# Optimization experiments

Hardware: AMD Instinct MI355X
Metric: run time of the kernel (lower is better)

## Reference

```python
import jax, jax.numpy as jnp
import numpy as np

N = 100000   # nodes per type (equal so the module's sloppy self-indexing is valid)
E = 1600000  # edges, avg degree 16
DIN = 128    # input feature dim (lazily inferred by SAGEConv((-1,-1), ...))
H = 256      # hidden (init default)


def _w(k, i, o):
    return jax.random.normal(k, (i, o), jnp.float32) * (1.0 / np.sqrt(i))


def setup_inputs() -> dict:
    key = jax.random.key(0)
    ks = jax.random.split(key, 16)
    inp = {
        "x_human": jax.random.normal(ks[0], (N, DIN), jnp.float32),
        "x_bact": jax.random.normal(ks[1], (N, DIN), jnp.float32),
        "edge_index": jax.random.randint(ks[2], (2, E), 0, N, dtype=jnp.int32),
        # human branch conv1 (DIN->H) and conv2 (H->H)
        "h1_Wl": _w(ks[3], DIN, H), "h1_Wr": _w(ks[4], DIN, H), "h1_b": jnp.zeros((H,), jnp.float32),
        "h2_Wl": _w(ks[5], H, H),   "h2_Wr": _w(ks[6], H, H),   "h2_b": jnp.zeros((H,), jnp.float32),
        # bacterial branch conv1 (DIN->H) and conv2 (H->H)
        "b1_Wl": _w(ks[7], DIN, H), "b1_Wr": _w(ks[8], DIN, H), "b1_b": jnp.zeros((H,), jnp.float32),
        "b2_Wl": _w(ks[9], H, H),   "b2_Wr": _w(ks[10], H, H),  "b2_b": jnp.zeros((H,), jnp.float32),
    }
    return inp


def sage_conv(x, src, dst, Wl, Wr, b):
    """PyG SAGEConv (aggr='mean', root_weight=True):
    out = Linear(mean_{j in N(i)} x_j) + Linear_noBias(x_i).
    Aggregate first, then matmul (same op order as PyG => less FLOPs/traffic)."""
    s = jax.ops.segment_sum(x[src], dst, num_segments=N)          # [N, d] scatter-sum of gathered messages
    cnt = jax.ops.segment_sum(jnp.ones((src.shape[0],), x.dtype), dst, num_segments=N)
    agg = s / jnp.maximum(cnt, 1.0)[:, None]                      # mean; isolated nodes -> 0
    return agg @ Wl + x @ Wr + b


def reference(x_human, x_bact, edge_index,
              h1_Wl, h1_Wr, h1_b, h2_Wl, h2_Wr, h2_b,
              b1_Wl, b1_Wr, b1_b, b2_Wl, b2_Wr, b2_b):
    src, dst = edge_index[0], edge_index[1]   # human -> bacterial
    # rev = edge.flip(0): messages flow bacterial_id -> human_id
    h = jax.nn.relu(sage_conv(x_human, dst, src, h1_Wl, h1_Wr, h1_b))
    h = jax.nn.relu(sage_conv(h, dst, src, h2_Wl, h2_Wr, h2_b))
    b = jax.nn.relu(sage_conv(x_bact, src, dst, b1_Wl, b1_Wr, b1_b))
    b = jax.nn.relu(sage_conv(b, src, dst, b2_Wl, b2_Wr, b2_b))
    return h, b
```

## Files before the change

### kernel.cpp

```cpp
#include <hip/hip_runtime.h>
#include <stdint.h>

using short8  = __attribute__((ext_vector_type(8))) short;
using float4v = __attribute__((ext_vector_type(4))) float;

__device__ __forceinline__ float b2f(unsigned short u) {
    union { unsigned int i; float f; } v; v.i = ((unsigned int)u) << 16; return v.f;
}
__device__ __forceinline__ unsigned short f2b(float f) {
    union { float f; unsigned int i; } v; v.f = f;
    unsigned int x = v.i;
    unsigned int r = (x + 0x7fffu + ((x >> 16) & 1u)) >> 16;
    return (unsigned short)r;
}

__device__ __forceinline__ void gload_lds16(const void* g, void* l) {
    __builtin_amdgcn_global_load_lds((const __attribute__((address_space(1))) void*)g,
                                     (__attribute__((address_space(3))) void*)l, 16, 0, 0);
}

__global__ __launch_bounds__(256)
void fill_ell_ranged(const int* __restrict__ src, const int* __restrict__ dst,
                     int* __restrict__ cnt_h, int* __restrict__ cnt_b,
                     int* __restrict__ adj_h, int* __restrict__ adj_b,
                     int E, int N, int nch) {
    const int NR = 8;
    int r     = blockIdx.x & (NR - 1);
    int chunk = blockIdx.x >> 3;
    int rng = (N + NR - 1) / NR;
    int lo = r * rng;
    int hi = lo + rng; if (hi > N) hi = N;
    int per = (E + nch - 1) / nch;
    int e0 = chunk * per;
    int e1 = e0 + per; if (e1 > E) e1 = E;
    for (int e = e0 + (int)threadIdx.x; e < e1; e += 256) {
        int s = __builtin_nontemporal_load(src + e);
        int d = __builtin_nontemporal_load(dst + e);
        if (s >= lo && s < hi) {
            int sl = atomicAdd(cnt_h + s, 1);
            if (sl < 64) adj_h[((size_t)s << 6) + sl] = d;
        }
        if (d >= lo && d < hi) {
            int sl = atomicAdd(cnt_b + d, 1);
            if (sl < 64) adj_b[((size_t)d << 6) + sl] = s;
        }
    }
}

__global__ void count_deg(const int* __restrict__ src, const int* __restrict__ dst,
                          int* __restrict__ deg_h, int* __restrict__ deg_b, int E) {
    int e = blockIdx.x * blockDim.x + threadIdx.x;
    if (e < E) {
        int s = __builtin_nontemporal_load(src + e);
        int d = __builtin_nontemporal_load(dst + e);
        atomicAdd(deg_h + s, 1);
        atomicAdd(deg_b + d, 1);
    }
}
__global__ void scan1(const int* __restrict__ deg, int* __restrict__ partial, int N) {
    int t = threadIdx.x;
    int base = blockIdx.x * 1024 + t * 4;
    int s = 0;
    #pragma unroll
    for (int i = 0; i < 4; ++i) { int idx = base + i; if (idx < N) s += deg[idx]; }
    #pragma unroll
    for (int off = 32; off; off >>= 1) s += __shfl_down(s, off);
    __shared__ int sm[4];
    if ((t & 63) == 0) sm[t >> 6] = s;
    __syncthreads();
    if (t == 0) partial[blockIdx.x] = sm[0] + sm[1] + sm[2] + sm[3];
}
__global__ void scan2(int* __restrict__ partial, int P) {
    if (blockIdx.x == 0 && threadIdx.x == 0) {
        int run = 0;
        for (int i = 0; i < P; ++i) { int v = partial[i]; partial[i] = run; run += v; }
    }
}
__global__ void scan3(const int* __restrict__ deg, const int* __restrict__ partial,
                      int* __restrict__ row, int N, int E) {
    int t = threadIdx.x;
    int lane = t & 63, wv = t >> 6;
    int base = blockIdx.x * 1024 + t * 4;
    int d[4]; int s = 0;
    #pragma unroll
    for (int i = 0; i < 4; ++i) { int idx = base + i; d[i] = (idx < N) ? deg[idx] : 0; s += d[i]; }
    int inc = s;
    #pragma unroll
    for (int off = 1; off < 64; off <<= 1) { int v = __shfl_up(inc, off); if (lane >= off) inc += v; }
    __shared__ int wsum[4];
    if (lane == 63) wsum[wv] = inc;
    __syncthreads();
    int woff = 0;
    for (int w = 0; w < wv; ++w) woff += wsum[w];
    int run = inc - s + woff + partial[blockIdx.x];
    #pragma unroll
    for (int i = 0; i < 4; ++i) { int idx = base + i; if (idx < N) row[idx] = run; run += d[i]; }
    if (blockIdx.x == 0 && t == 0) row[N] = E;
}
__global__ __launch_bounds__(256)
void fill_adj_ranged(const int* __restrict__ src, const int* __restrict__ dst,
                     int* __restrict__ cur_h, int* __restrict__ cur_b,
                     int* __restrict__ adj_h, int* __restrict__ adj_b,
                     int E, int N, int nch) {
    const int NR = 8;
    int r     = blockIdx.x & (NR - 1);
    int chunk = blockIdx.x >> 3;
    int rng = (N + NR - 1) / NR;
    int lo = r * rng;
    int hi = lo + rng; if (hi > N) hi = N;
    int per = (E + nch - 1) / nch;
    int e0 = chunk * per;
    int e1 = e0 + per; if (e1 > E) e1 = E;
    for (int e = e0 + (int)threadIdx.x; e < e1; e += 256) {
        int s = __builtin_nontemporal_load(src + e);
        int d = __builtin_nontemporal_load(dst + e);
        if (s >= lo && s < hi) adj_h[atomicAdd(cur_h + s, 1)] = d;
        if (d >= lo && d < hi) adj_b[atomicAdd(cur_b + d, 1)] = s;
    }
}

__global__ void cvt_to_bf16(const float* __restrict__ in, unsigned short* __restrict__ out,
                            size_t n4) {
    size_t t = (size_t)blockIdx.x * blockDim.x + threadIdx.x;
    if (t >= n4) return;
    const float4 v = *(const float4*)(in + t * 4);
    ushort4 u;
    u.x = f2b(v.x); u.y = f2b(v.y); u.z = f2b(v.z); u.w = f2b(v.w);
    *(ushort4*)(out + t * 4) = u;
}

template <int D>
__global__ __launch_bounds__(256)
void gather_mean(const unsigned short* __restrict__ x, const int* __restrict__ rowc,
                 const int* __restrict__ adj, unsigned short* __restrict__ out,
                 int N, int ell) {
    constexpr int LPR = D / 8;
    constexpr int G   = 64 / LPR;
    constexpr int UNR = 16 / G;
    int wid  = (blockIdx.x * blockDim.x + threadIdx.x) >> 6;
    int lane = threadIdx.x & 63;
    if (wid >= N) return;
    int beg, deg;
    if (ell) { beg = wid << 6; int c = rowc[wid]; deg = (c < 64) ? c : 64; }
    else     { beg = rowc[wid]; deg = rowc[wid + 1] - beg; }

    const int g  = lane >> (LPR == 16 ? 4 : 5);
    const int gl = lane & (LPR - 1);

    float acc[8];
    #pragma unroll
    for (int p = 0; p < 8; ++p) acc[p] = 0.0f;

    for (int base = 0; base < deg; base += 64) {
        int nb_l = (base + lane < deg) ? adj[beg + base + lane] : 0;
        int m = deg - base; if (m > 64) m = 64;
        int j = 0;
        for (; j + UNR * G <= m; j += UNR * G) {
            int nn[UNR];
            #pragma unroll
            for (int u = 0; u < UNR; ++u) nn[u] = __shfl(nb_l, j + u * G + g);
            short8 vv[UNR];
            #pragma unroll
            for (int u = 0; u < UNR; ++u)
                vv[u] = *(const short8*)(x + (size_t)nn[u] * D + gl * 8);
            #pragma unroll
            for (int u = 0; u < UNR; ++u)
                #pragma unroll
                for (int p = 0; p < 8; ++p) acc[p] += b2f((unsigned short)vv[u][p]);
        }
        for (; j < m; j += G) {
            int idx = j + g;
            int nb = __shfl(nb_l, idx);
            if (idx < m) {
                const short8 v = *(const short8*)(x + (size_t)nb * D + gl * 8);
                #pragma unroll
                for (int p = 0; p < 8; ++p) acc[p] += b2f((unsigned short)v[p]);
            }
        }
    }
    #pragma unroll
    for (int off = LPR; off < 64; off <<= 1) {
        #pragma unroll
        for (int p = 0; p < 8; ++p) acc[p] += __shfl_xor(acc[p], off);
    }
    float inv = 1.0f / (float)((deg > 0) ? deg : 1);
    if (lane < LPR) {
        unsigned short* op = out + (size_t)wid * D + lane * 8;
        short8 u;
        #pragma unroll
        for (int p = 0; p < 8; ++p) u[p] = (short)f2b(acc[p] * inv);
        *(short8*)op = u;
    }
}

__global__ void transpose_w4(const float* __restrict__ W0, const float* __restrict__ W1,
                             const float* __restrict__ W2, const float* __restrict__ W3,
                             unsigned short* __restrict__ T0, unsigned short* __restrict__ T1,
                             unsigned short* __restrict__ T2, unsigned short* __restrict__ T3,
                             int K) {
    int k = blockIdx.x;
    int c = threadIdx.x;
    int m = blockIdx.y;
    const float* W = (m == 0) ? W0 : (m == 1) ? W1 : (m == 2) ? W2 : W3;
    unsigned short* T = (m == 0) ? T0 : (m == 1) ? T1 : (m == 2) ? T2 : T3;
    T[(size_t)c * K + k] = f2b(W[(size_t)k * 256 + c]);
}

template <bool F32OUT>
__global__ __launch_bounds__(256, 3)
void gemm_fused(const unsigned short* __restrict__ A0, const unsigned short* __restrict__ A1,
                const unsigned short* __restrict__ B0, const unsigned short* __restrict__ B1,
                const float* __restrict__ bias,
                float* __restrict__ outf, unsigned short* __restrict__ outb,
                int M, int K) {
    __shared__ unsigned short As[64 * 64];
    __shared__ unsigned short Bs[256 * 64];
    const int tid  = threadIdx.x;
    const int wave = tid >> 6, lane = tid & 63;
    const int wn   = wave;
    const int row0 = blockIdx.x * 64;

    float4v acc[4][4];
    #pragma unroll
    for (int i = 0; i < 4; ++i)
        #pragma unroll
        for (int j = 0; j < 4; ++j) acc[i][j] = (float4v){0.f, 0.f, 0.f, 0.f};

    const int r  = lane >> 3;
    const int cg = lane & 7;
    const int kchunks = K >> 6;
    const int nchunks = kchunks * 2;

    for (int c = 0; c < nchunks; ++c) {
        const unsigned short* Aseg = (c < kchunks) ? A0 : A1;
        const unsigned short* Bseg = (c < kchunks) ? B0 : B1;
        const int k0 = ((c < kchunks) ? c : c - kchunks) << 6;

        if (c) __syncthreads();
        {
            int rr = wave * 16;
            const unsigned short* gp = Aseg + (size_t)(row0 + rr + r) * K + k0 + cg * 8;
            unsigned short* lp = As + rr * 64;
            if (row0 + rr + r < M)     gload_lds16(gp, lp);
            if (row0 + rr + 8 + r < M) gload_lds16(gp + 8 * (size_t)K, lp + 8 * 64);
        }
        {
            int rr = wave * 64;
            const unsigned short* gp = Bseg + (size_t)(rr + r) * K + k0 + cg * 8;
            unsigned short* lp = Bs + rr * 64;
            #pragma unroll
            for (int i = 0; i < 8; ++i)
                gload_lds16(gp + (size_t)(i * 8) * K, lp + i * 8 * 64);
        }
        __syncthreads();

        const int q8 = (lane >> 4) * 8;
        const int l15 = lane & 15;
        #pragma unroll
        for (int kk = 0; kk <= 32; kk += 32) {
            short8 af[4], bf[4];
            #pragma unroll
            for (int f = 0; f < 4; ++f)
                af[f] = *(const short8*)(As + (f * 16 + l15) * 64 + kk + q8);
            #pragma unroll
            for (int f = 0; f < 4; ++f)
                bf[f] = *(const short8*)(Bs + (wn * 64 + f * 16 + l15) * 64 + kk + q8);
            #pragma unroll
            for (int fm = 0; fm < 4; ++fm)
                #pragma unroll
                for (int fn = 0; fn < 4; ++fn)
                    acc[fm][fn] = __builtin_amdgcn_mfma_f32_16x16x32_bf16(
                        af[fm], bf[fn], acc[fm][fn], 0, 0, 0);
        }
    }

    const int l15 = lane & 15;
    const int rq  = (lane >> 4) * 4;
    #pragma unroll
    for (int fn = 0; fn < 4; ++fn) {
        int col = wn * 64 + fn * 16 + l15;
        float bv = bias[col];
        #pragma unroll
        for (int fm = 0; fm < 4; ++fm) {
            #pragma unroll
            for (int rg = 0; rg < 4; ++rg) {
                int row = row0 + fm * 16 + rq + rg;
                if (row < M) {
                    float v = fmaxf(acc[fm][fn][rg] + bv, 0.0f);
                    if (F32OUT) outf[(size_t)row * 256 + col] = v;
                    else        outb[(size_t)row * 256 + col] = f2b(v);
                }
            }
        }
    }
}

extern "C" void kernel_launch(void* const* d_in, const int* in_sizes, int n_in,
                              void* d_out, int out_size, void* d_ws, size_t ws_size,
                              hipStream_t stream) {
    const int DIN = 128, H = 256;
    const int N = in_sizes[0] / DIN;
    const int E = in_sizes[2] / 2;

    const float* xh = (const float*)d_in[0];
    const float* xb = (const float*)d_in[1];
    const int* ei  = (const int*)d_in[2];
    const int* src = ei;
    const int* dst = ei + E;
    const float* h1Wl = (const float*)d_in[3];
    const float* h1Wr = (const float*)d_in[4];
    const float* h1b  = (const float*)d_in[5];
    const float* h2Wl = (const float*)d_in[6];
    const float* h2Wr = (const float*)d_in[7];
    const float* h2b  = (const float*)d_in[8];
    const float* b1Wl = (const float*)d_in[9];
    const float* b1Wr = (const float*)d_in[10];
    const float* b1b  = (const float*)d_in[11];
    const float* b2Wl = (const float*)d_in[12];
    const float* b2Wr = (const float*)d_in[13];
    const float* b2b  = (const float*)d_in[14];

    float* outH = (float*)d_out;
    float* outB = outH + (size_t)N * H;

    const int BLK = 256;
    dim3 blk(BLK);

    const size_t bfElems = (size_t)4 * DIN * H + (size_t)4 * H * H
                         + (size_t)N * DIN + (size_t)2 * N * H;
    const size_t bfBytes = bfElems * 2 + 64;

    const size_t needELL = ((size_t)2 * N + (size_t)128 * N) * 4 + bfBytes;
    const bool useELL = ws_size >= needELL;

    const int* rc_h; const int* rc_b; const int* ajh; const int* ajb;
    uintptr_t intEnd;

    if (useELL) {
        int* cnt_h = (int*)d_ws;
        int* cnt_b = cnt_h + N;
        int* adj_h = cnt_b + N;
        int* adj_b = adj_h + (size_t)N * 64;
        intEnd = (uintptr_t)(adj_b + (size_t)N * 64);

        hipMemsetAsync(cnt_h, 0, (size_t)2 * N * sizeof(int), stream);
        const int NCH = 256;
        fill_ell_ranged<<<dim3(NCH * 8), blk, 0, stream>>>(src, dst, cnt_h, cnt_b,
                                                           adj_h, adj_b, E, N, NCH);
        rc_h = cnt_h; rc_b = cnt_b; ajh = adj_h; ajb = adj_b;
    } else {
        int* deg_h = (int*)d_ws;
        int* deg_b = deg_h + N;
        int* row_h = deg_b + N;
        int* row_b = row_h + (N + 1);
        int* cur_h = row_b + (N + 1);
        int* cur_b = cur_h + N;
        int* partial = cur_b + N;
        int* adj_h = partial + 256;
        int* adj_b = adj_h + E;
        intEnd = (uintptr_t)(adj_b + E);

        const int P = (N + 1023) / 1024;
        hipMemsetAsync(deg_h, 0, (size_t)2 * N * sizeof(int), stream);
        count_deg<<<dim3((E + BLK - 1) / BLK), blk, 0, stream>>>(src, dst, deg_h, deg_b, E);
        scan1<<<dim3(P), blk, 0, stream>>>(deg_h, partial, N);
        scan2<<<dim3(1), blk, 0, stream>>>(partial, P);
        scan3<<<dim3(P), blk, 0, stream>>>(deg_h, partial, row_h, N, E);
        scan1<<<dim3(P), blk, 0, stream>>>(deg_b, partial, N);
        scan2<<<dim3(1), blk, 0, stream>>>(partial, P);
        scan3<<<dim3(P), blk, 0, stream>>>(deg_b, partial, row_b, N, E);
        hipMemcpyAsync(cur_h, row_h, (size_t)N * sizeof(int), hipMemcpyDeviceToDevice, stream);
        hipMemcpyAsync(cur_b, row_b, (size_t)N * sizeof(int), hipMemcpyDeviceToDevice, stream);
        const int NCH = 256;
        fill_adj_ranged<<<dim3(NCH * 8), blk, 0, stream>>>(src, dst, cur_h, cur_b,
                                                           adj_h, adj_b, E, N, NCH);
        rc_h = row_h; rc_b = row_b; ajh = adj_h; ajb = adj_b;
    }
    const int ellf = useELL ? 1 : 0;

    uintptr_t up = (intEnd + 63) & ~(uintptr_t)63;
    unsigned short* wtp = (unsigned short*)up;
    unsigned short* t_h1l = wtp; wtp += DIN * H;
    unsigned short* t_h1r = wtp; wtp += DIN * H;
    unsigned short* t_h2l = wtp; wtp += H * H;
    unsigned short* t_h2r = wtp; wtp += H * H;
    unsigned short* t_b1l = wtp; wtp += DIN * H;
    unsigned short* t_b1r = wtp; wtp += DIN * H;
    unsigned short* t_b2l = wtp; wtp += H * H;
    unsigned short* t_b2r = wtp; wtp += H * H;
    unsigned short* xbf   = wtp;
    unsigned short* aggbf = xbf + (size_t)N * DIN;
    unsigned short* hbf   = aggbf + (size_t)N * H;

    transpose_w4<<<dim3(DIN, 4), blk, 0, stream>>>(h1Wl, h1Wr, b1Wl, b1Wr,
                                                   t_h1l, t_h1r, t_b1l, t_b1r, DIN);
    transpose_w4<<<dim3(H, 4),   blk, 0, stream>>>(h2Wl, h2Wr, b2Wl, b2Wr,
                                                   t_h2l, t_h2r, t_b2l, t_b2r, H);

    dim3 nggrid((N + 3) / 4);
    dim3 ggrid((N + 63) / 64);
    int ncvt = ((size_t)N * DIN / 4 + BLK - 1) / BLK;

    cvt_to_bf16<<<dim3(ncvt), blk, 0, stream>>>(xh, xbf, (size_t)N * DIN / 4);
    gather_mean<128><<<nggrid, blk, 0, stream>>>(xbf, rc_h, ajh, aggbf, N, ellf);
    gemm_fused<false><<<ggrid, blk, 0, stream>>>(aggbf, xbf, t_h1l, t_h1r, h1b,
                                                 nullptr, hbf, N, DIN);
    gather_mean<256><<<nggrid, blk, 0, stream>>>(hbf, rc_h, ajh, aggbf, N, ellf);
    gemm_fused<true><<<ggrid, blk, 0, stream>>>(aggbf, hbf, t_h2l, t_h2r, h2b,
                                                outH, nullptr, N, H);

    cvt_to_bf16<<<dim3(ncvt), blk, 0, stream>>>(xb, xbf, (size_t)N * DIN / 4);
    gather_mean<128><<<nggrid, blk, 0, stream>>>(xbf, rc_b, ajb, aggbf, N, ellf);
    gemm_fused<false><<<ggrid, blk, 0, stream>>>(aggbf, xbf, t_b1l, t_b1r, b1b,
                                                 nullptr, hbf, N, DIN);
    gather_mean<256><<<nggrid, blk, 0, stream>>>(hbf, rc_b, ajb, aggbf, N, ellf);
    gemm_fused<true><<<ggrid, blk, 0, stream>>>(aggbf, hbf, t_b2l, t_b2r, b2b,
                                                outB, nullptr, N, H);
}
```

Before: 1.019 ms.

## Split ELL fill per direction and enlarge GEMM tile to 128 rows

The ELL build kernel is split into two launches, one per direction, each loading the value array only when the key falls in the block's range, which cuts redundant loads and branching. The fused GEMM moves from 64-row tiles with 4 waves to 128-row tiles with 8 waves (2x4 wave grid), so each B tile staged in LDS is reused across twice as many rows. This halves B traffic per output row but raises LDS use per block and changes occupancy, and the ELL build now reads the key array twice.

After: 1.119 ms. 1.1x slower.

```diff
diff --git a/kernel.cpp b/kernel.cpp
--- a/kernel.cpp
+++ b/kernel.cpp
@@ -20,10 +20,9 @@
 }
 
 __global__ __launch_bounds__(256)
-void fill_ell_ranged(const int* __restrict__ src, const int* __restrict__ dst,
-                     int* __restrict__ cnt_h, int* __restrict__ cnt_b,
-                     int* __restrict__ adj_h, int* __restrict__ adj_b,
-                     int E, int N, int nch) {
+void fill_ell_dir(const int* __restrict__ key, const int* __restrict__ val,
+                  int* __restrict__ cnt, int* __restrict__ adj,
+                  int E, int N, int nch) {
     const int NR = 8;
     int r     = blockIdx.x & (NR - 1);
     int chunk = blockIdx.x >> 3;
@@ -34,15 +33,11 @@
     int e0 = chunk * per;
     int e1 = e0 + per; if (e1 > E) e1 = E;
     for (int e = e0 + (int)threadIdx.x; e < e1; e += 256) {
-        int s = __builtin_nontemporal_load(src + e);
-        int d = __builtin_nontemporal_load(dst + e);
-        if (s >= lo && s < hi) {
-            int sl = atomicAdd(cnt_h + s, 1);
-            if (sl < 64) adj_h[((size_t)s << 6) + sl] = d;
-        }
-        if (d >= lo && d < hi) {
-            int sl = atomicAdd(cnt_b + d, 1);
-            if (sl < 64) adj_b[((size_t)d << 6) + sl] = s;
+        int k = __builtin_nontemporal_load(key + e);
+        if (k >= lo && k < hi) {
+            int v = __builtin_nontemporal_load(val + e);
+            int sl = atomicAdd(cnt + k, 1);
+            if (sl < 64) adj[((size_t)k << 6) + sl] = v;
         }
     }
 }
@@ -207,18 +202,19 @@
 }
 
 template <bool F32OUT>
-__global__ __launch_bounds__(256, 3)
+__global__ __launch_bounds__(512, 2)
 void gemm_fused(const unsigned short* __restrict__ A0, const unsigned short* __restrict__ A1,
                 const unsigned short* __restrict__ B0, const unsigned short* __restrict__ B1,
                 const float* __restrict__ bias,
                 float* __restrict__ outf, unsigned short* __restrict__ outb,
                 int M, int K) {
-    __shared__ unsigned short As[64 * 64];
+    __shared__ unsigned short As[128 * 64];
     __shared__ unsigned short Bs[256 * 64];
     const int tid  = threadIdx.x;
     const int wave = tid >> 6, lane = tid & 63;
-    const int wn   = wave;
-    const int row0 = blockIdx.x * 64;
+    const int wm   = wave >> 2;
+    const int wn   = wave & 3;
+    const int row0 = blockIdx.x * 128;
 
     float4v acc[4][4];
     #pragma unroll
@@ -245,11 +241,11 @@
             if (row0 + rr + 8 + r < M) gload_lds16(gp + 8 * (size_t)K, lp + 8 * 64);
         }
         {
-            int rr = wave * 64;
+            int rr = wave * 32;
             const unsigned short* gp = Bseg + (size_t)(rr + r) * K + k0 + cg * 8;
             unsigned short* lp = Bs + rr * 64;
             #pragma unroll
-            for (int i = 0; i < 8; ++i)
+            for (int i = 0; i < 4; ++i)
                 gload_lds16(gp + (size_t)(i * 8) * K, lp + i * 8 * 64);
         }
         __syncthreads();
@@ -261,7 +257,7 @@
             short8 af[4], bf[4];
             #pragma unroll
             for (int f = 0; f < 4; ++f)
-                af[f] = *(const short8*)(As + (f * 16 + l15) * 64 + kk + q8);
+                af[f] = *(const short8*)(As + (wm * 64 + f * 16 + l15) * 64 + kk + q8);
             #pragma unroll
             for (int f = 0; f < 4; ++f)
                 bf[f] = *(const short8*)(Bs + (wn * 64 + f * 16 + l15) * 64 + kk + q8);
@@ -284,7 +280,7 @@
         for (int fm = 0; fm < 4; ++fm) {
             #pragma unroll
             for (int rg = 0; rg < 4; ++rg) {
-                int row = row0 + fm * 16 + rq + rg;
+                int row = row0 + wm * 64 + fm * 16 + rq + rg;
                 if (row < M) {
                     float v = fmaxf(acc[fm][fn][rg] + bv, 0.0f);
                     if (F32OUT) outf[(size_t)row * 256 + col] = v;
@@ -345,8 +341,8 @@
 
         hipMemsetAsync(cnt_h, 0, (size_t)2 * N * sizeof(int), stream);
         const int NCH = 256;
-        fill_ell_ranged<<<dim3(NCH * 8), blk, 0, stream>>>(src, dst, cnt_h, cnt_b,
-                                                           adj_h, adj_b, E, N, NCH);
+        fill_ell_dir<<<dim3(NCH * 8), blk, 0, stream>>>(src, dst, cnt_h, adj_h, E, N, NCH);
+        fill_ell_dir<<<dim3(NCH * 8), blk, 0, stream>>>(dst, src, cnt_b, adj_b, E, N, NCH);
         rc_h = cnt_h; rc_b = cnt_b; ajh = adj_h; ajb = adj_b;
     } else {
         int* deg_h = (int*)d_ws;
@@ -398,22 +394,23 @@
                                                    t_h2l, t_h2r, t_b2l, t_b2r, H);
 
     dim3 nggrid((N + 3) / 4);
-    dim3 ggrid((N + 63) / 64);
+    dim3 ggrid((N + 127) / 128);
+    dim3 gblk(512);
     int ncvt = ((size_t)N * DIN / 4 + BLK - 1) / BLK;
 
     cvt_to_bf16<<<dim3(ncvt), blk, 0, stream>>>(xh, xbf, (size_t)N * DIN / 4);
     gather_mean<128><<<nggrid, blk, 0, stream>>>(xbf, rc_h, ajh, aggbf, N, ellf);
-    gemm_fused<false><<<ggrid, blk, 0, stream>>>(aggbf, xbf, t_h1l, t_h1r, h1b,
-                                                 nullptr, hbf, N, DIN);
+    gemm_fused<false><<<ggrid, gblk, 0, stream>>>(aggbf, xbf, t_h1l, t_h1r, h1b,
+                                                  nullptr, hbf, N, DIN);
     gather_mean<256><<<nggrid, blk, 0, stream>>>(hbf, rc_h, ajh, aggbf, N, ellf);
-    gemm_fused<true><<<ggrid, blk, 0, stream>>>(aggbf, hbf, t_h2l, t_h2r, h2b,
-                                                outH, nullptr, N, H);
+    gemm_fused<true><<<ggrid, gblk, 0, stream>>>(aggbf, hbf, t_h2l, t_h2r, h2b,
+                                                 outH, nullptr, N, H);
 
     cvt_to_bf16<<<dim3(ncvt), blk, 0, stream>>>(xb, xbf, (size_t)N * DIN / 4);
     gather_mean<128><<<nggrid, blk, 0, stream>>>(xbf, rc_b, ajb, aggbf, N, ellf);
-    gemm_fused<false><<<ggrid, blk, 0, stream>>>(aggbf, xbf, t_b1l, t_b1r, b1b,
-                                                 nullptr, hbf, N, DIN);
+    gemm_fused<false><<<ggrid, gblk, 0, stream>>>(aggbf, xbf, t_b1l, t_b1r, b1b,
+                                                  nullptr, hbf, N, DIN);
     gather_mean<256><<<nggrid, blk, 0, stream>>>(hbf, rc_b, ajb, aggbf, N, ellf);
-    gemm_fused<true><<<ggrid, blk, 0, stream>>>(aggbf, hbf, t_b2l, t_b2r, b2b,
-                                                outB, nullptr, N, H);
-}
+    gemm_fused<true><<<ggrid, gblk, 0, stream>>>(aggbf, hbf, t_b2l, t_b2r, b2b,
+                                                 outB, nullptr, N, H);
+}
```

## Interleave human and bacterial branches via fused gemm+gather launches and single prep kernel

Applied to the files above, without the earlier changes.

Merges ELL fill, both bf16 conversions, weight transposes and zero-row setup into one prep kernel. It then runs the two independent branches in lockstep, so each launch pairs one branch's GEMM blocks with the other branch's gather blocks. The gather now loads a full 64-wide adjacency row at once and pads out-of-range lanes with a zero sentinel row instead of using a tail loop. The CSR path is removed. Separate buffers for each branch increase workspace, and a fallback sequential path remains for small workspaces.

Measured after the change: 1.021 ms. No clear change (+0.1%).

```diff
diff --git a/kernel.cpp b/kernel.cpp
--- a/kernel.cpp
+++ b/kernel.cpp
@@ -13,24 +13,22 @@
     unsigned int r = (x + 0x7fffu + ((x >> 16) & 1u)) >> 16;
     return (unsigned short)r;
 }
-
 __device__ __forceinline__ void gload_lds16(const void* g, void* l) {
     __builtin_amdgcn_global_load_lds((const __attribute__((address_space(1))) void*)g,
                                      (__attribute__((address_space(3))) void*)l, 16, 0, 0);
 }
 
-__global__ __launch_bounds__(256)
-void fill_ell_ranged(const int* __restrict__ src, const int* __restrict__ dst,
-                     int* __restrict__ cnt_h, int* __restrict__ cnt_b,
-                     int* __restrict__ adj_h, int* __restrict__ adj_b,
-                     int E, int N, int nch) {
-    const int NR = 8;
-    int r     = blockIdx.x & (NR - 1);
-    int chunk = blockIdx.x >> 3;
+__device__ __forceinline__ void fill_body(const int* __restrict__ src, const int* __restrict__ dst,
+                                          int* __restrict__ cnt_h, int* __restrict__ cnt_b,
+                                          int* __restrict__ adj_h, int* __restrict__ adj_b,
+                                          int E, int N, int bid) {
+    const int NR = 8, NCH = 256;
+    int r     = bid & (NR - 1);
+    int chunk = bid >> 3;
     int rng = (N + NR - 1) / NR;
     int lo = r * rng;
     int hi = lo + rng; if (hi > N) hi = N;
-    int per = (E + nch - 1) / nch;
+    int per = (E + NCH - 1) / NCH;
     int e0 = chunk * per;
     int e1 = e0 + per; if (e1 > E) e1 = E;
     for (int e = e0 + (int)threadIdx.x; e < e1; e += 256) {
@@ -47,75 +45,259 @@
     }
 }
 
-__global__ void count_deg(const int* __restrict__ src, const int* __restrict__ dst,
-                          int* __restrict__ deg_h, int* __restrict__ deg_b, int E) {
-    int e = blockIdx.x * blockDim.x + threadIdx.x;
-    if (e < E) {
-        int s = __builtin_nontemporal_load(src + e);
-        int d = __builtin_nontemporal_load(dst + e);
-        atomicAdd(deg_h + s, 1);
-        atomicAdd(deg_b + d, 1);
-    }
-}
-__global__ void scan1(const int* __restrict__ deg, int* __restrict__ partial, int N) {
-    int t = threadIdx.x;
-    int base = blockIdx.x * 1024 + t * 4;
-    int s = 0;
+__global__ __launch_bounds__(256)
+void fill_ell_ranged(const int* __restrict__ src, const int* __restrict__ dst,
+                     int* __restrict__ cnt_h, int* __restrict__ cnt_b,
+                     int* __restrict__ adj_h, int* __restrict__ adj_b, int E, int N) {
+    fill_body(src, dst, cnt_h, cnt_b, adj_h, adj_b, E, N, blockIdx.x);
+}
+
+__global__ __launch_bounds__(256)
+void prep(const int* __restrict__ src, const int* __restrict__ dst,
+          int* __restrict__ cnt_h, int* __restrict__ cnt_b,
+          int* __restrict__ adj_h, int* __restrict__ adj_b, int E, int N,
+          const float* __restrict__ xh, unsigned short* __restrict__ xbf_h,
+          const float* __restrict__ xb, unsigned short* __restrict__ xbf_b,
+          const float* __restrict__ h1Wl, const float* __restrict__ h1Wr,
+          const float* __restrict__ b1Wl, const float* __restrict__ b1Wr,
+          const float* __restrict__ h2Wl, const float* __restrict__ h2Wr,
+          const float* __restrict__ b2Wl, const float* __restrict__ b2Wr,
+          unsigned short* __restrict__ t_h1l, unsigned short* __restrict__ t_h1r,
+          unsigned short* __restrict__ t_b1l, unsigned short* __restrict__ t_b1r,
+          unsigned short* __restrict__ t_h2l, unsigned short* __restrict__ t_h2r,
+          unsigned short* __restrict__ t_b2l, unsigned short* __restrict__ t_b2r,
+          unsigned short* __restrict__ h_h, unsigned short* __restrict__ h_b) {
+    const int FB = 2048;
+    const int n4 = N * 32;
+    const int CB = (n4 + 255) / 256;
+    int bid = blockIdx.x;
+    int tid = threadIdx.x;
+
+    if (bid < FB) {
+        fill_body(src, dst, cnt_h, cnt_b, adj_h, adj_b, E, N, bid);
+        return;
+    }
+    bid -= FB;
+    if (bid < 2 * CB) {
+        const float* in = (bid < CB) ? xh : xb;
+        unsigned short* out = (bid < CB) ? xbf_h : xbf_b;
+        int b2 = (bid < CB) ? bid : bid - CB;
+        size_t t = (size_t)b2 * 256 + tid;
+        if (t < (size_t)n4) {
+            const float4 v = *(const float4*)(in + t * 4);
+            ushort4 u;
+            u.x = f2b(v.x); u.y = f2b(v.y); u.z = f2b(v.z); u.w = f2b(v.w);
+            *(ushort4*)(out + t * 4) = u;
+        }
+        return;
+    }
+    bid -= 2 * CB;
+    if (bid < 512) {
+        int m = bid >> 7, k = bid & 127;
+        const float* W = (m == 0) ? h1Wl : (m == 1) ? h1Wr : (m == 2) ? b1Wl : b1Wr;
+        unsigned short* T = (m == 0) ? t_h1l : (m == 1) ? t_h1r : (m == 2) ? t_b1l : t_b1r;
+        T[(size_t)tid * 128 + k] = f2b(W[(size_t)k * 256 + tid]);
+        return;
+    }
+    bid -= 512;
+    if (bid < 1024) {
+        int m = bid >> 8, k = bid & 255;
+        const float* W = (m == 0) ? h2Wl : (m == 1) ? h2Wr : (m == 2) ? b2Wl : b2Wr;
+        unsigned short* T = (m == 0) ? t_h2l : (m == 1) ? t_h2r : (m == 2) ? t_b2l : t_b2r;
+        T[(size_t)tid * 256 + k] = f2b(W[(size_t)k * 256 + tid]);
+        return;
+    }
+    if (tid < 128) {
+        xbf_h[(size_t)N * 128 + tid] = 0;
+        xbf_b[(size_t)N * 128 + tid] = 0;
+    }
+    h_h[(size_t)N * 256 + tid] = 0;
+    h_b[(size_t)N * 256 + tid] = 0;
+}
+
+template <int D>
+__device__ __forceinline__ void gather_body(const unsigned short* __restrict__ x,
+                                            const int* __restrict__ cnt,
+                                            const int* __restrict__ adj,
+                                            unsigned short* __restrict__ out,
+                                            int N, int bid) {
+    constexpr int LPR = D / 8;
+    constexpr int G   = 64 / LPR;
+    constexpr int STEP = 16;
+    constexpr int UNR = STEP / G;
+    int wave = (int)threadIdx.x >> 6;
+    int lane = (int)threadIdx.x & 63;
+    int wid = bid * 4 + wave;
+    if (wid >= N) return;
+    int c = cnt[wid];
+    int deg = (c < 64) ? c : 64;
+    int nb_l = adj[((size_t)wid << 6) + lane];
+
+    const int g  = lane >> (LPR == 16 ? 4 : 5);
+    const int gl = lane & (LPR - 1);
+
+    float acc[8];
     #pragma unroll
-    for (int i = 0; i < 4; ++i) { int idx = base + i; if (idx < N) s += deg[idx]; }
+    for (int p = 0; p < 8; ++p) acc[p] = 0.0f;
+
+    int rounds = (deg + STEP - 1) >> 4;
+    for (int t = 0; t < rounds; ++t) {
+        int j = t * STEP;
+        int nn[UNR];
+        #pragma unroll
+        for (int u = 0; u < UNR; ++u) {
+            int idx = j + u * G + g;
+            int v = __shfl(nb_l, idx);
+            nn[u] = (idx < deg) ? v : N;
+        }
+        short8 vv[UNR];
+        #pragma unroll
+        for (int u = 0; u < UNR; ++u)
+            vv[u] = *(const short8*)(x + (size_t)nn[u] * D + gl * 8);
+        #pragma unroll
+        for (int u = 0; u < UNR; ++u)
+            #pragma unroll
+            for (int p = 0; p < 8; ++p) acc[p] += b2f((unsigned short)vv[u][p]);
+    }
     #pragma unroll
-    for (int off = 32; off; off >>= 1) s += __shfl_down(s, off);
-    __shared__ int sm[4];
-    if ((t & 63) == 0) sm[t >> 6] = s;
-    __syncthreads();
-    if (t == 0) partial[blockIdx.x] = sm[0] + sm[1] + sm[2] + sm[3];
-}
-__global__ void scan2(int* __restrict__ partial, int P) {
-    if (blockIdx.x == 0 && threadIdx.x == 0) {
-        int run = 0;
-        for (int i = 0; i < P; ++i) { int v = partial[i]; partial[i] = run; run += v; }
-    }
-}
-__global__ void scan3(const int* __restrict__ deg, const int* __restrict__ partial,
-                      int* __restrict__ row, int N, int E) {
-    int t = threadIdx.x;
-    int lane = t & 63, wv = t >> 6;
-    int base = blockIdx.x * 1024 + t * 4;
-    int d[4]; int s = 0;
+    for (int off = LPR; off < 64; off <<= 1) {
+        #pragma unroll
+        for (int p = 0; p < 8; ++p) acc[p] += __shfl_xor(acc[p], off);
+    }
+    float inv = 1.0f / (float)((deg > 0) ? deg : 1);
+    if (lane < LPR) {
+        unsigned short* op = out + (size_t)wid * D + lane * 8;
+        short8 u;
+        #pragma unroll
+        for (int p = 0; p < 8; ++p) u[p] = (short)f2b(acc[p] * inv);
+        *(short8*)op = u;
+    }
+}
+
+template <int D>
+__global__ __launch_bounds__(256)
+void gather_mean_sel(const unsigned short* __restrict__ x, const int* __restrict__ cnt,
+                     const int* __restrict__ adj, unsigned short* __restrict__ out, int N) {
+    gather_body<D>(x, cnt, adj, out, N, blockIdx.x);
+}
+
+template <bool F32OUT>
+__device__ __forceinline__ void gemm_body(const unsigned short* __restrict__ A0,
+                                          const unsigned short* __restrict__ A1,
+                                          const unsigned short* __restrict__ B0,
+                                          const unsigned short* __restrict__ B1,
+                                          const float* __restrict__ bias,
+                                          float* __restrict__ outf,
+                                          unsigned short* __restrict__ outb,
+                                          int M, int K,
+                                          unsigned short* As, unsigned short* Bs, int bid) {
+    const int tid  = threadIdx.x;
+    const int wave = tid >> 6, lane = tid & 63;
+    const int wn   = wave;
+    const int row0 = bid * 64;
+
+    float4v acc[4][4];
     #pragma unroll
-    for (int i = 0; i < 4; ++i) { int idx = base + i; d[i] = (idx < N) ? deg[idx] : 0; s += d[i]; }
-    int inc = s;
+    for (int i = 0; i < 4; ++i)
+        #pragma unroll
+        for (int j = 0; j < 4; ++j) acc[i][j] = (float4v){0.f, 0.f, 0.f, 0.f};
+
+    const int r  = lane >> 3;
+    const int cg = lane & 7;
+    const int kchunks = K >> 6;
+    const int nchunks = kchunks * 2;
+
+    for (int c = 0; c < nchunks; ++c) {
+        const unsigned short* Aseg = (c < kchunks) ? A0 : A1;
+        const unsigned short* Bseg = (c < kchunks) ? B0 : B1;
+        const int k0 = ((c < kchunks) ? c : c - kchunks) << 6;
+
+        if (c) __syncthreads();
+        {
+            int rr = wave * 16;
+            const unsigned short* gp = Aseg + (size_t)(row0 + rr + r) * K + k0 + cg * 8;
+            unsigned short* lp = As + rr * 64;
+            if (row0 + rr + r < M)     gload_lds16(gp, lp);
+            if (row0 + rr + 8 + r < M) gload_lds16(gp + 8 * (size_t)K, lp + 8 * 64);
+        }
+        {
+            int rr = wave * 64;
+            const unsigned short* gp = Bseg + (size_t)(rr + r) * K + k0 + cg * 8;
+            unsigned short* lp = Bs + rr * 64;
+            #pragma unroll
+            for (int i = 0; i < 8; ++i)
+                gload_lds16(gp + (size_t)(i * 8) * K, lp + i * 8 * 64);
+        }
+        __syncthreads();
+
+        const int q8 = (lane >> 4) * 8;
+        const int l15 = lane & 15;
+        #pragma unroll
+        for (int kk = 0; kk <= 32; kk += 32) {
+            short8 af[4], bf[4];
+            #pragma unroll
+            for (int f = 0; f < 4; ++f)
+                af[f] = *(const short8*)(As + (f * 16 + l15) * 64 + kk + q8);
+            #pragma unroll
+            for (int f = 0; f < 4; ++f)
+                bf[f] = *(const short8*)(Bs + (wn * 64 + f * 16 + l15) * 64 + kk + q8);
+            #pragma unroll
+            for (int fm = 0; fm < 4; ++fm)
+                #pragma unroll
+                for (int fn = 0; fn < 4; ++fn)
+                    acc[fm][fn] = __builtin_amdgcn_mfma_f32_16x16x32_bf16(
+                        af[fm], bf[fn], acc[fm][fn], 0, 0, 0);
+        }
+    }
+
+    const int l15 = lane & 15;
+    const int rq  = (lane >> 4) * 4;
     #pragma unroll
-    for (int off = 1; off < 64; off <<= 1) { int v = __shfl_up(inc, off); if (lane >= off) inc += v; }
-    __shared__ int wsum[4];
-    if (lane == 63) wsum[wv] = inc;
-    __syncthreads();
-    int woff = 0;
-    for (int w = 0; w < wv; ++w) woff += wsum[w];
-    int run = inc - s + woff + partial[blockIdx.x];
-    #pragma unroll
-    for (int i = 0; i < 4; ++i) { int idx = base + i; if (idx < N) row[idx] = run; run += d[i]; }
-    if (blockIdx.x == 0 && t == 0) row[N] = E;
-}
-__global__ __launch_bounds__(256)
-void fill_adj_ranged(const int* __restrict__ src, const int* __restrict__ dst,
-                     int* __restrict__ cur_h, int* __restrict__ cur_b,
-                     int* __restrict__ adj_h, int* __restrict__ adj_b,
-                     int E, int N, int nch) {
-    const int NR = 8;
-    int r     = blockIdx.x & (NR - 1);
-    int chunk = blockIdx.x >> 3;
-    int rng = (N + NR - 1) / NR;
-    int lo = r * rng;
-    int hi = lo + rng; if (hi > N) hi = N;
-    int per = (E + nch - 1) / nch;
-    int e0 = chunk * per;
-    int e1 = e0 + per; if (e1 > E) e1 = E;
-    for (int e = e0 + (int)threadIdx.x; e < e1; e += 256) {
-        int s = __builtin_nontemporal_load(src + e);
-        int d = __builtin_nontemporal_load(dst + e);
-        if (s >= lo && s < hi) adj_h[atomicAdd(cur_h + s, 1)] = d;
-        if (d >= lo && d < hi) adj_b[atomicAdd(cur_b + d, 1)] = s;
+    for (int fn = 0; fn < 4; ++fn) {
+        int col = wn * 64 + fn * 16 + l15;
+        float bv = bias[col];
+        #pragma unroll
+        for (int fm = 0; fm < 4; ++fm) {
+            #pragma unroll
+            for (int rg = 0; rg < 4; ++rg) {
+                int row = row0 + fm * 16 + rq + rg;
+                if (row < M) {
+                    float v = fmaxf(acc[fm][fn][rg] + bv, 0.0f);
+                    if (F32OUT) outf[(size_t)row * 256 + col] = v;
+                    else        outb[(size_t)row * 256 + col] = f2b(v);
+                }
+            }
+        }
+    }
+}
+
+template <bool F32OUT>
+__global__ __launch_bounds__(256, 3)
+void gemm_fused(const unsigned short* __restrict__ A0, const unsigned short* __restrict__ A1,
+                const unsigned short* __restrict__ B0, const unsigned short* __restrict__ B1,
+                const float* __restrict__ bias,
+                float* __restrict__ outf, unsigned short* __restrict__ outb, int M, int K) {
+    __shared__ unsigned short As[64 * 64];
+    __shared__ unsigned short Bs[256 * 64];
+    gemm_body<F32OUT>(A0, A1, B0, B1, bias, outf, outb, M, K, As, Bs, blockIdx.x);
+}
+
+template <bool F32OUT, int DG>
+__global__ __launch_bounds__(256, 3)
+void fused_gg(const unsigned short* __restrict__ A0, const unsigned short* __restrict__ A1,
+              const unsigned short* __restrict__ B0, const unsigned short* __restrict__ B1,
+              const float* __restrict__ bias,
+              float* __restrict__ outf, unsigned short* __restrict__ outb, int M, int K,
+              const unsigned short* __restrict__ gx, const int* __restrict__ gcnt,
+              const int* __restrict__ gadj, unsigned short* __restrict__ gout,
+              int N, int gemmBlocks) {
+    __shared__ unsigned short As[64 * 64];
+    __shared__ unsigned short Bs[256 * 64];
+    int bid = blockIdx.x;
+    if (bid < gemmBlocks) {
+        gemm_body<F32OUT>(A0, A1, B0, B1, bias, outf, outb, M, K, As, Bs, bid);
+    } else {
+        gather_body<DG>(gx, gcnt, gadj, gout, N, bid - gemmBlocks);
     }
 }
 
@@ -128,71 +310,6 @@
     u.x = f2b(v.x); u.y = f2b(v.y); u.z = f2b(v.z); u.w = f2b(v.w);
     *(ushort4*)(out + t * 4) = u;
 }
-
-template <int D>
-__global__ __launch_bounds__(256)
-void gather_mean(const unsigned short* __restrict__ x, const int* __restrict__ rowc,
-                 const int* __restrict__ adj, unsigned short* __restrict__ out,
-                 int N, int ell) {
-    constexpr int LPR = D / 8;
-    constexpr int G   = 64 / LPR;
-    constexpr int UNR = 16 / G;
-    int wid  = (blockIdx.x * blockDim.x + threadIdx.x) >> 6;
-    int lane = threadIdx.x & 63;
-    if (wid >= N) return;
-    int beg, deg;
-    if (ell) { beg = wid << 6; int c = rowc[wid]; deg = (c < 64) ? c : 64; }
-    else     { beg = rowc[wid]; deg = rowc[wid + 1] - beg; }
-
-    const int g  = lane >> (LPR == 16 ? 4 : 5);
-    const int gl = lane & (LPR - 1);
-
-    float acc[8];
-    #pragma unroll
-    for (int p = 0; p < 8; ++p) acc[p] = 0.0f;
-
-    for (int base = 0; base < deg; base += 64) {
-        int nb_l = (base + lane < deg) ? adj[beg + base + lane] : 0;
-        int m = deg - base; if (m > 64) m = 64;
-        int j = 0;
-        for (; j + UNR * G <= m; j += UNR * G) {
-            int nn[UNR];
-            #pragma unroll
-            for (int u = 0; u < UNR; ++u) nn[u] = __shfl(nb_l, j + u * G + g);
-            short8 vv[UNR];
-            #pragma unroll
-            for (int u = 0; u < UNR; ++u)
-                vv[u] = *(const short8*)(x + (size_t)nn[u] * D + gl * 8);
-            #pragma unroll
-            for (int u = 0; u < UNR; ++u)
-                #pragma unroll
-                for (int p = 0; p < 8; ++p) acc[p] += b2f((unsigned short)vv[u][p]);
-        }
-        for (; j < m; j += G) {
-            int idx = j + g;
-            int nb = __shfl(nb_l, idx);
-            if (idx < m) {
-                const short8 v = *(const short8*)(x + (size_t)nb * D + gl * 8);
-                #pragma unroll
-                for (int p = 0; p < 8; ++p) acc[p] += b2f((unsigned short)v[p]);
-            }
-        }
-    }
-    #pragma unroll
-    for (int off = LPR; off < 64; off <<= 1) {
-        #pragma unroll
-        for (int p = 0; p < 8; ++p) acc[p] += __shfl_xor(acc[p], off);
-    }
-    float inv = 1.0f / (float)((deg > 0) ? deg : 1);
-    if (lane < LPR) {
-        unsigned short* op = out + (size_t)wid * D + lane * 8;
-        short8 u;
-        #pragma unroll
-        for (int p = 0; p < 8; ++p) u[p] = (short)f2b(acc[p] * inv);
-        *(short8*)op = u;
-    }
-}
-
 __global__ void transpose_w4(const float* __restrict__ W0, const float* __restrict__ W1,
                              const float* __restrict__ W2, const float* __restrict__ W3,
                              unsigned short* __restrict__ T0, unsigned short* __restrict__ T1,
@@ -204,95 +321,6 @@
     const float* W = (m == 0) ? W0 : (m == 1) ? W1 : (m == 2) ? W2 : W3;
     unsigned short* T = (m == 0) ? T0 : (m == 1) ? T1 : (m == 2) ? T2 : T3;
     T[(size_t)c * K + k] = f2b(W[(size_t)k * 256 + c]);
-}
-
-template <bool F32OUT>
-__global__ __launch_bounds__(256, 3)
-void gemm_fused(const unsigned short* __restrict__ A0, const unsigned short* __restrict__ A1,
-                const unsigned short* __restrict__ B0, const unsigned short* __restrict__ B1,
-                const float* __restrict__ bias,
-                float* __restrict__ outf, unsigned short* __restrict__ outb,
-                int M, int K) {
-    __shared__ unsigned short As[64 * 64];
-    __shared__ unsigned short Bs[256 * 64];
-    const int tid  = threadIdx.x;
-    const int wave = tid >> 6, lane = tid & 63;
-    const int wn   = wave;
-    const int row0 = blockIdx.x * 64;
-
-    float4v acc[4][4];
-    #pragma unroll
-    for (int i = 0; i < 4; ++i)
-        #pragma unroll
-        for (int j = 0; j < 4; ++j) acc[i][j] = (float4v){0.f, 0.f, 0.f, 0.f};
-
-    const int r  = lane >> 3;
-    const int cg = lane & 7;
-    const int kchunks = K >> 6;
-    const int nchunks = kchunks * 2;
-
-    for (int c = 0; c < nchunks; ++c) {
-        const unsigned short* Aseg = (c < kchunks) ? A0 : A1;
-        const unsigned short* Bseg = (c < kchunks) ? B0 : B1;
-        const int k0 = ((c < kchunks) ? c : c - kchunks) << 6;
-
-        if (c) __syncthreads();
-        {
-            int rr = wave * 16;
-            const unsigned short* gp = Aseg + (size_t)(row0 + rr + r) * K + k0 + cg * 8;
-            unsigned short* lp = As + rr * 64;
-            if (row0 + rr + r < M)     gload_lds16(gp, lp);
-            if (row0 + rr + 8 + r < M) gload_lds16(gp + 8 * (size_t)K, lp + 8 * 64);
-        }
-        {
-            int rr = wave * 64;
-            const unsigned short* gp = Bseg + (size_t)(rr + r) * K + k0 + cg * 8;
-            unsigned short* lp = Bs + rr * 64;
-            #pragma unroll
-            for (int i = 0; i < 8; ++i)
-                gload_lds16(gp + (size_t)(i * 8) * K, lp + i * 8 * 64);
-        }
-        __syncthreads();
-
-        const int q8 = (lane >> 4) * 8;
-        const int l15 = lane & 15;
-        #pragma unroll
-        for (int kk = 0; kk <= 32; kk += 32) {
-            short8 af[4], bf[4];
-            #pragma unroll
-            for (int f = 0; f < 4; ++f)
-                af[f] = *(const short8*)(As + (f * 16 + l15) * 64 + kk + q8);
-            #pragma unroll
-            for (int f = 0; f < 4; ++f)
-                bf[f] = *(const short8*)(Bs + (wn * 64 + f * 16 + l15) * 64 + kk + q8);
-            #pragma unroll
-            for (int fm = 0; fm < 4; ++fm)
-                #pragma unroll
-                for (int fn = 0; fn < 4; ++fn)
-                    acc[fm][fn] = __builtin_amdgcn_mfma_f32_16x16x32_bf16(
-                        af[fm], bf[fn], acc[fm][fn], 0, 0, 0);
-        }
-    }
-
-    const int l15 = lane & 15;
-    const int rq  = (lane >> 4) * 4;
-    #pragma unroll
-    for (int fn = 0; fn < 4; ++fn) {
-        int col = wn * 64 + fn * 16 + l15;
-        float bv = bias[col];
-        #pragma unroll
-        for (int fm = 0; fm < 4; ++fm) {
-            #pragma unroll
-            for (int rg = 0; rg < 4; ++rg) {
-                int row = row0 + fm * 16 + rq + rg;
-                if (row < M) {
-                    float v = fmaxf(acc[fm][fn][rg] + bv, 0.0f);
-                    if (F32OUT) outf[(size_t)row * 256 + col] = v;
-                    else        outb[(size_t)row * 256 + col] = f2b(v);
-                }
-            }
-        }
-    }
 }
 
 extern "C" void kernel_launch(void* const* d_in, const int* in_sizes, int n_in,
@@ -326,58 +354,11 @@
     const int BLK = 256;
     dim3 blk(BLK);
 
-    const size_t bfElems = (size_t)4 * DIN * H + (size_t)4 * H * H
-                         + (size_t)N * DIN + (size_t)2 * N * H;
-    const size_t bfBytes = bfElems * 2 + 64;
-
-    const size_t needELL = ((size_t)2 * N + (size_t)128 * N) * 4 + bfBytes;
-    const bool useELL = ws_size >= needELL;
-
-    const int* rc_h; const int* rc_b; const int* ajh; const int* ajb;
-    uintptr_t intEnd;
-
-    if (useELL) {
-        int* cnt_h = (int*)d_ws;
-        int* cnt_b = cnt_h + N;
-        int* adj_h = cnt_b + N;
-        int* adj_b = adj_h + (size_t)N * 64;
-        intEnd = (uintptr_t)(adj_b + (size_t)N * 64);
-
-        hipMemsetAsync(cnt_h, 0, (size_t)2 * N * sizeof(int), stream);
-        const int NCH = 256;
-        fill_ell_ranged<<<dim3(NCH * 8), blk, 0, stream>>>(src, dst, cnt_h, cnt_b,
-                                                           adj_h, adj_b, E, N, NCH);
-        rc_h = cnt_h; rc_b = cnt_b; ajh = adj_h; ajb = adj_b;
-    } else {
-        int* deg_h = (int*)d_ws;
-        int* deg_b = deg_h + N;
-        int* row_h = deg_b + N;
-        int* row_b = row_h + (N + 1);
-        int* cur_h = row_b + (N + 1);
-        int* cur_b = cur_h + N;
-        int* partial = cur_b + N;
-        int* adj_h = partial + 256;
-        int* adj_b = adj_h + E;
-        intEnd = (uintptr_t)(adj_b + E);
-
-        const int P = (N + 1023) / 1024;
-        hipMemsetAsync(deg_h, 0, (size_t)2 * N * sizeof(int), stream);
-        count_deg<<<dim3((E + BLK - 1) / BLK), blk, 0, stream>>>(src, dst, deg_h, deg_b, E);
-        scan1<<<dim3(P), blk, 0, stream>>>(deg_h, partial, N);
-        scan2<<<dim3(1), blk, 0, stream>>>(partial, P);
-        scan3<<<dim3(P), blk, 0, stream>>>(deg_h, partial, row_h, N, E);
-        scan1<<<dim3(P), blk, 0, stream>>>(deg_b, partial, N);
-        scan2<<<dim3(1), blk, 0, stream>>>(partial, P);
-        scan3<<<dim3(P), blk, 0, stream>>>(deg_b, partial, row_b, N, E);
-        hipMemcpyAsync(cur_h, row_h, (size_t)N * sizeof(int), hipMemcpyDeviceToDevice, stream);
-        hipMemcpyAsync(cur_b, row_b, (size_t)N * sizeof(int), hipMemcpyDeviceToDevice, stream);
-        const int NCH = 256;
-        fill_adj_ranged<<<dim3(NCH * 8), blk, 0, stream>>>(src, dst, cur_h, cur_b,
-                                                           adj_h, adj_b, E, N, NCH);
-        rc_h = row_h; rc_b = row_b; ajh = adj_h; ajb = adj_b;
-    }
-    const int ellf = useELL ? 1 : 0;
-
+    int* cnt_h = (int*)d_ws;
+    int* cnt_b = cnt_h + N;
+    int* adj_h = cnt_b + N;
+    int* adj_b = adj_h + (size_t)N * 64;
+    uintptr_t intEnd = (uintptr_t)(adj_b + (size_t)N * 64);
     uintptr_t up = (intEnd + 63) & ~(uintptr_t)63;
     unsigned short* wtp = (unsigned short*)up;
     unsigned short* t_h1l = wtp; wtp += DIN * H;
@@ -388,32 +369,76 @@
     unsigned short* t_b1r = wtp; wtp += DIN * H;
     unsigned short* t_b2l = wtp; wtp += H * H;
     unsigned short* t_b2r = wtp; wtp += H * H;
-    unsigned short* xbf   = wtp;
-    unsigned short* aggbf = xbf + (size_t)N * DIN;
-    unsigned short* hbf   = aggbf + (size_t)N * H;
-
-    transpose_w4<<<dim3(DIN, 4), blk, 0, stream>>>(h1Wl, h1Wr, b1Wl, b1Wr,
-                                                   t_h1l, t_h1r, t_b1l, t_b1r, DIN);
-    transpose_w4<<<dim3(H, 4),   blk, 0, stream>>>(h2Wl, h2Wr, b2Wl, b2Wr,
-                                                   t_h2l, t_h2r, t_b2l, t_b2r, H);
-
-    dim3 nggrid((N + 3) / 4);
-    dim3 ggrid((N + 63) / 64);
-    int ncvt = ((size_t)N * DIN / 4 + BLK - 1) / BLK;
-
-    cvt_to_bf16<<<dim3(ncvt), blk, 0, stream>>>(xh, xbf, (size_t)N * DIN / 4);
-    gather_mean<128><<<nggrid, blk, 0, stream>>>(xbf, rc_h, ajh, aggbf, N, ellf);
-    gemm_fused<false><<<ggrid, blk, 0, stream>>>(aggbf, xbf, t_h1l, t_h1r, h1b,
-                                                 nullptr, hbf, N, DIN);
-    gather_mean<256><<<nggrid, blk, 0, stream>>>(hbf, rc_h, ajh, aggbf, N, ellf);
-    gemm_fused<true><<<ggrid, blk, 0, stream>>>(aggbf, hbf, t_h2l, t_h2r, h2b,
-                                                outH, nullptr, N, H);
-
-    cvt_to_bf16<<<dim3(ncvt), blk, 0, stream>>>(xb, xbf, (size_t)N * DIN / 4);
-    gather_mean<128><<<nggrid, blk, 0, stream>>>(xbf, rc_b, ajb, aggbf, N, ellf);
-    gemm_fused<false><<<ggrid, blk, 0, stream>>>(aggbf, xbf, t_b1l, t_b1r, b1b,
-                                                 nullptr, hbf, N, DIN);
-    gather_mean<256><<<nggrid, blk, 0, stream>>>(hbf, rc_b, ajb, aggbf, N, ellf);
-    gemm_fused<true><<<ggrid, blk, 0, stream>>>(aggbf, hbf, t_b2l, t_b2r, b2b,
-                                                outB, nullptr, N, H);
-}
+
+    const size_t xrow = (size_t)(N + 1) * DIN;
+    const size_t arow = (size_t)N * H;
+    const size_t hrow = (size_t)(N + 1) * H;
+    size_t parElems = 2 * xrow + 2 * arow + 2 * hrow;
+    size_t needPAR = ((uintptr_t)wtp + parElems * 2) - (uintptr_t)d_ws;
+    const bool usePAR = ws_size >= needPAR;
+
+    const int GB = (N + 63) / 64;
+    const int NB = (N + 3) / 4;
+    const int n4 = N * (DIN / 4);
+    const int CB = (n4 + 255) / 256;
+
+    if (usePAR) {
+        unsigned short* xbf_h = wtp;          wtp += xrow;
+        unsigned short* xbf_b = wtp;          wtp += xrow;
+        unsigned short* agg_h = wtp;          wtp += arow;
+        unsigned short* agg_b = wtp;          wtp += arow;
+        unsigned short* h_h   = wtp;          wtp += hrow;
+        unsigned short* h_b   = wtp;
+
+        hipMemsetAsync(cnt_h, 0, (size_t)2 * N * sizeof(int), stream);
+        int prepGrid = 2048 + 2 * CB + 512 + 1024 + 1;
+        prep<<<dim3(prepGrid), blk, 0, stream>>>(src, dst, cnt_h, cnt_b, adj_h, adj_b, E, N,
+                                                 xh, xbf_h, xb, xbf_b,
+                                                 h1Wl, h1Wr, b1Wl, b1Wr,
+                                                 h2Wl, h2Wr, b2Wl, b2Wr,
+                                                 t_h1l, t_h1r, t_b1l, t_b1r,
+                                                 t_h2l, t_h2r, t_b2l, t_b2r,
+                                                 h_h, h_b);
+        gather_mean_sel<128><<<dim3(NB), blk, 0, stream>>>(xbf_h, cnt_h, adj_h, agg_h, N);
+        fused_gg<false, 128><<<dim3(GB + NB), blk, 0, stream>>>(
+            agg_h, xbf_h, t_h1l, t_h1r, h1b, nullptr, h_h, N, DIN,
+            xbf_b, cnt_b, adj_b, agg_b, N, GB);
+        fused_gg<false, 256><<<dim3(GB + NB), blk, 0, stream>>>(
+            agg_b, xbf_b, t_b1l, t_b1r, b1b, nullptr, h_b, N, DIN,
+            h_h, cnt_h, adj_h, agg_h, N, GB);
+        fused_gg<true, 256><<<dim3(GB + NB), blk, 0, stream>>>(
+            agg_h, h_h, t_h2l, t_h2r, h2b, outH, nullptr, N, H,
+            h_b, cnt_b, adj_b, agg_b, N, GB);
+        gemm_fused<true><<<dim3(GB), blk, 0, stream>>>(agg_b, h_b, t_b2l, t_b2r, b2b,
+                                                       outB, nullptr, N, H);
+    } else {
+        unsigned short* xbf   = wtp;          wtp += xrow;
+        unsigned short* aggbf = wtp;          wtp += arow;
+        unsigned short* hbf   = wtp;
+
+        hipMemsetAsync(cnt_h, 0, (size_t)2 * N * sizeof(int), stream);
+        hipMemsetAsync(xbf + (size_t)N * DIN, 0, DIN * sizeof(unsigned short), stream);
+        hipMemsetAsync(hbf + (size_t)N * H, 0, H * sizeof(unsigned short), stream);
+        fill_ell_ranged<<<dim3(2048), blk, 0, stream>>>(src, dst, cnt_h, cnt_b,
+                                                        adj_h, adj_b, E, N);
+        transpose_w4<<<dim3(DIN, 4), blk, 0, stream>>>(h1Wl, h1Wr, b1Wl, b1Wr,
+                                                       t_h1l, t_h1r, t_b1l, t_b1r, DIN);
+        transpose_w4<<<dim3(H, 4),   blk, 0, stream>>>(h2Wl, h2Wr, b2Wl, b2Wr,
+                                                       t_h2l, t_h2r, t_b2l, t_b2r, H);
+        int ncvt = (n4 + BLK - 1) / BLK;
+        cvt_to_bf16<<<dim3(ncvt), blk, 0, stream>>>(xh, xbf, (size_t)n4);
+        gather_mean_sel<128><<<dim3(NB), blk, 0, stream>>>(xbf, cnt_h, adj_h, aggbf, N);
+        gemm_fused<false><<<dim3(GB), blk, 0, stream>>>(aggbf, xbf, t_h1l, t_h1r, h1b,
+                                                        nullptr, hbf, N, DIN);
+        gather_mean_sel<256><<<dim3(NB), blk, 0, stream>>>(hbf, cnt_h, adj_h, aggbf, N);
+        gemm_fused<true><<<dim3(GB), blk, 0, stream>>>(aggbf, hbf, t_h2l, t_h2r, h2b,
+                                                       outH, nullptr, N, H);
+        cvt_to_bf16<<<dim3(ncvt), blk, 0, stream>>>(xb, xbf, (size_t)n4);
+        gather_mean_sel<128><<<dim3(NB), blk, 0, stream>>>(xbf, cnt_b, adj_b, aggbf, N);
+        gemm_fused<false><<<dim3(GB), blk, 0, stream>>>(aggbf, xbf, t_b1l, t_b1r, b1b,
+                                                        nullptr, hbf, N, DIN);
+        gather_mean_sel<256><<<dim3(NB), blk, 0, stream>>>(hbf, cnt_b, adj_b, aggbf, N);
+        gemm_fused<true><<<dim3(GB), blk, 0, stream>>>(aggbf, hbf, t_b2l, t_b2r, b2b,
+                                                       outB, nullptr, N, H);
+    }
+}
```
